# Kernel tuning notes

Measured on AMD Instinct MI355X. Metric: run time of the kernel, lower is better.

Reference implementation:

```python
import jax, jax.numpy as jnp
import numpy as np

B, S, D, H, FF = 4, 2048, 512, 8, 2048
W = 128  # local attention window size (hardcoded in module)
DH = D // H


def _ln(x, g, b, eps=1e-5):
    m = x.mean(-1, keepdims=True)
    v = ((x - m) ** 2).mean(-1, keepdims=True)
    return (x - m) / jnp.sqrt(v + eps) * g + b


def setup_inputs() -> dict:
    key = jax.random.key(0)
    ks = jax.random.split(key, 10)
    s = 0.02
    return {
        "src": jax.random.normal(ks[0], (B, S, D), jnp.float32),
        # global nn.MultiheadAttention params
        "in_proj_w": jax.random.normal(ks[1], (3 * D, D), jnp.float32) * s,
        "in_proj_b": jnp.zeros((3 * D,), jnp.float32),
        "out_proj_w": jax.random.normal(ks[2], (D, D), jnp.float32) * s,
        "out_proj_b": jnp.zeros((D,), jnp.float32),
        # LocalMHA params (prenorm LN, fused qkv no-bias, out proj no-bias)
        "ln_g": jnp.ones((D,), jnp.float32),
        "ln_b": jnp.zeros((D,), jnp.float32),
        "qkv_w": jax.random.normal(ks[3], (3 * D, D), jnp.float32) * s,
        "to_out_w": jax.random.normal(ks[4], (D, D), jnp.float32) * s,
        # glFusion + FFN + norms
        "gl_w": jax.random.normal(ks[5], (D, 2 * D), jnp.float32) * s,
        "gl_b": jnp.zeros((D,), jnp.float32),
        "norm1_g": jnp.ones((D,), jnp.float32),
        "norm1_b": jnp.zeros((D,), jnp.float32),
        "lin1_w": jax.random.normal(ks[6], (FF, D), jnp.float32) * s,
        "lin1_b": jnp.zeros((FF,), jnp.float32),
        "lin2_w": jax.random.normal(ks[7], (D, FF), jnp.float32) * s,
        "lin2_b": jnp.zeros((D,), jnp.float32),
        "norm2_g": jnp.ones((D,), jnp.float32),
        "norm2_b": jnp.zeros((D,), jnp.float32),
    }


def _forward(src, in_proj_w, in_proj_b, out_proj_w, out_proj_b, ln_g, ln_b,
             qkv_w, to_out_w, gl_w, gl_b, norm1_g, norm1_b,
             lin1_w, lin1_b, lin2_w, lin2_b, norm2_g, norm2_b):
    b, s, d = src.shape
    scale = DH ** -0.5

    def heads(x):  # (b, s, d) -> (b, H, s, DH)
        return x.reshape(b, s, H, DH).transpose(0, 2, 1, 3)

    # ---- global full MHA (no mask) ----
    qkv = src @ in_proj_w.T + in_proj_b
    qg, kg, vg = (heads(t) for t in jnp.split(qkv, 3, axis=-1))
    att = jax.nn.softmax(jnp.einsum('bhid,bhjd->bhij', qg, kg) * scale, axis=-1)
    go = jnp.einsum('bhij,bhjd->bhid', att, vg).transpose(0, 2, 1, 3).reshape(b, s, d)
    go = go @ out_proj_w.T + out_proj_b

    # ---- local windowed causal MHA with rotary (window=128, look_backward=1) ----
    x = _ln(src, ln_g, ln_b)  # prenorm
    ql, kl, vl = (heads(t) for t in jnp.split(x @ qkv_w.T, 3, axis=-1))

    pos = jnp.arange(s)
    inv_freq = 1.0 / (10000.0 ** (jnp.arange(0, DH, 2, dtype=jnp.float32) / DH))
    freqs = pos[:, None].astype(jnp.float32) * inv_freq[None, :]
    emb = jnp.concatenate([freqs, freqs], axis=-1)  # (s, DH)
    cos, sin = jnp.cos(emb), jnp.sin(emb)

    def rope(t):
        h = DH // 2
        t1, t2 = t[..., :h], t[..., h:]
        return t * cos + jnp.concatenate([-t2, t1], axis=-1) * sin

    ql, kl = rope(ql), rope(kl)
    ql = ql * scale

    nw = s // W
    qw = ql.reshape(b, H, nw, W, DH)
    kw = kl.reshape(b, H, nw, W, DH)
    vw = vl.reshape(b, H, nw, W, DH)

    def look_back(t):  # concat previous window with current: (b,H,nw,2W,DH)
        prev = jnp.pad(t, ((0, 0), (0, 0), (1, 0), (0, 0), (0, 0)))[:, :, :-1]
        return jnp.concatenate([prev, t], axis=3)

    bk, bv = look_back(kw), look_back(vw)

    qpos = pos.reshape(nw, W)
    kpos = jnp.concatenate(
        [jnp.concatenate([jnp.full((1, W), -1, pos.dtype), qpos[:-1]], axis=0), qpos],
        axis=1)  # (nw, 2W)
    mask = (kpos[:, None, :] >= 0) & (kpos[:, None, :] <= qpos[:, :, None])  # (nw,W,2W)

    sc = jnp.einsum('bhnid,bhnjd->bhnij', qw, bk)
    sc = jnp.where(mask, sc, jnp.finfo(sc.dtype).min)
    at = jax.nn.softmax(sc, axis=-1)
    lo = jnp.einsum('bhnij,bhnjd->bhnid', at, bv).reshape(b, H, s, DH)
    lo = lo.transpose(0, 2, 1, 3).reshape(b, s, d) @ to_out_w.T

    # ---- fuse global+local, residual, norms, FFN ----
    src2 = jnp.concatenate([go, lo], axis=-1) @ gl_w.T + gl_b
    h1 = _ln(src + src2, norm1_g, norm1_b)
    ff = jax.nn.relu(h1 @ lin1_w.T + lin1_b) @ lin2_w.T + lin2_b
    return _ln(h1 + ff, norm2_g, norm2_b)


def reference(src, in_proj_w, in_proj_b, out_proj_w, out_proj_b, ln_g, ln_b,
              qkv_w, to_out_w, gl_w, gl_b, norm1_g, norm1_b,
              lin1_w, lin1_b, lin2_w, lin2_b, norm2_g, norm2_b):
    return _forward(src, in_proj_w, in_proj_b, out_proj_w, out_proj_b, ln_g, ln_b,
                    qkv_w, to_out_w, gl_w, gl_b, norm1_g, norm1_b,
                    lin1_w, lin1_b, lin2_w, lin2_b, norm2_g, norm2_b)
```

## Files before the change

kernel.cpp:

```cpp
#include <hip/hip_runtime.h>
#include <math.h>

#define B_  4
#define S_  2048
#define D_  512
#define H_  8
#define FF_ 2048
#define W_  128
#define DH_ 64
#define TRD (3*D_)
#define MR_ (B_*S_)
#define QKLD 1024
#define SCQ 0.18033688011112042f

typedef __attribute__((ext_vector_type(8)))  short short8;
typedef __attribute__((ext_vector_type(4)))  float f32x4;
typedef __attribute__((ext_vector_type(16))) float f32x16;

__device__ __forceinline__ short f2bf(float f) {
    unsigned u = __float_as_uint(f);
    unsigned r = (u + 0x7fff + ((u >> 16) & 1)) >> 16;
    return (short)r;
}
__device__ __forceinline__ float bf2f(ushort u) {
    return __uint_as_float(((unsigned)u) << 16);
}
__device__ __forceinline__ unsigned pack_bf_trunc(float f0, float f1) {
    return __builtin_amdgcn_perm(__float_as_uint(f1), __float_as_uint(f0), 0x07060302u);
}
__device__ __forceinline__ void gload_lds16(const ushort* g, short* l) {
    __builtin_amdgcn_global_load_lds(
        (const __attribute__((address_space(1))) void*)g,
        (__attribute__((address_space(3))) void*)l, 16, 0, 0);
}

struct CvtJobs { const float* s[8]; ushort* d[8]; int n[8]; };

__global__ __launch_bounds__(256) void cvt_kernel(CvtJobs jobs)
{
    int i4 = (blockIdx.x * 256 + threadIdx.x) * 4;
    #pragma unroll
    for (int j = 0; j < 8; j++) {
        if (i4 < jobs.n[j]) {
            float4 v = *(const float4*)(jobs.s[j] + i4);
            ushort4 o;
            o.x = (ushort)f2bf(v.x); o.y = (ushort)f2bf(v.y);
            o.z = (ushort)f2bf(v.z); o.w = (ushort)f2bf(v.w);
            *(ushort4*)(jobs.d[j] + i4) = o;
        }
    }
}

__global__ __launch_bounds__(256) void gemm_bf16_kernel(
    const ushort* __restrict__ A, int lda,
    const ushort* __restrict__ Wt,
    const float* __restrict__ bias,
    ushort* __restrict__ C, int ldc,
    ushort* __restrict__ vt,
    int K, int relu)
{
    __shared__ short As[128 * 64];
    __shared__ short Bs[64 * 64];
    const int tid  = threadIdx.x;
    const int w    = tid >> 6;
    const int lane = tid & 63;
    const int quad = lane >> 4;
    const int x    = lane & 15;
    const int wr = w >> 1, wc = w & 1;
    const int bm = blockIdx.y * 128;
    const int bn = blockIdx.x * 64;

    const int srow = (lane >> 3);
    const int scol = ((lane & 7) ^ (lane >> 3)) * 8;

    f32x4 acc[4][2];
    #pragma unroll
    for (int i = 0; i < 4; i++)
        #pragma unroll
        for (int j = 0; j < 2; j++) acc[i][j] = (f32x4)0.f;

    for (int k0 = 0; k0 < K; k0 += 64) {
        __syncthreads();
        #pragma unroll
        for (int c = 0; c < 4; c++) {
            const ushort* ga = A + (size_t)(bm + w * 32 + c * 8 + srow) * lda + k0 + scol;
            gload_lds16(ga, &As[(w * 32 + c * 8) * 64]);
        }
        #pragma unroll
        for (int c = 0; c < 2; c++) {
            const ushort* gb = Wt + (size_t)(bn + w * 16 + c * 8 + srow) * K + k0 + scol;
            gload_lds16(gb, &Bs[(w * 16 + c * 8) * 64]);
        }
        __syncthreads();

        #pragma unroll
        for (int kc = 0; kc < 2; kc++) {
            short8 af[4], bf[2];
            int pcg = (kc * 4 + quad) ^ (x & 7);
            #pragma unroll
            for (int i = 0; i < 4; i++)
                af[i] = *(const short8*)&As[(wr * 64 + i * 16 + x) * 64 + pcg * 8];
            #pragma unroll
            for (int j = 0; j < 2; j++)
                bf[j] = *(const short8*)&Bs[(wc * 32 + j * 16 + x) * 64 + pcg * 8];
            #pragma unroll
            for (int i = 0; i < 4; i++)
                #pragma unroll
                for (int j = 0; j < 2; j++)
                    acc[i][j] = __builtin_amdgcn_mfma_f32_16x16x32_bf16(af[i], bf[j], acc[i][j], 0, 0, 0);
        }
    }

    if (vt) {
        #pragma unroll
        for (int i = 0; i < 4; i++) {
            int rowbase = bm + wr * 64 + i * 16 + quad * 4;
            #pragma unroll
            for (int j = 0; j < 2; j++) {
                int col = bn + wc * 32 + j * 16 + x;
                float bv = bias ? bias[col] : 0.f;
                if (col < 1024) {
                    #pragma unroll
                    for (int r = 0; r < 4; r++)
                        C[(size_t)(rowbase + r) * QKLD + col] = (ushort)f2bf(acc[i][j][r] + bv);
                } else {
                    int cv = col - 1024, hh = cv >> 6, dd = cv & 63;
                    int bb = rowbase >> 11, ss = rowbase & 2047;
                    int quadp = ((quad & 1) << 1) | (quad >> 1);
                    int sp = (ss & ~15) | (quadp << 2);
                    ushort4 p4;
                    p4.x = (ushort)f2bf(acc[i][j][0] + bv);
                    p4.y = (ushort)f2bf(acc[i][j][1] + bv);
                    p4.z = (ushort)f2bf(acc[i][j][2] + bv);
                    p4.w = (ushort)f2bf(acc[i][j][3] + bv);
                    *(ushort4*)(vt + ((size_t)((bb * 8 + hh) * 64 + dd)) * S_ + sp) = p4;
                }
            }
        }
    } else {
        #pragma unroll
        for (int i = 0; i < 4; i++) {
            #pragma unroll
            for (int r = 0; r < 4; r++) {
                size_t row = (size_t)(bm + wr * 64 + i * 16 + quad * 4 + r);
                #pragma unroll
                for (int j = 0; j < 2; j++) {
                    int col = bn + wc * 32 + j * 16 + x;
                    float v = acc[i][j][r] + (bias ? bias[col] : 0.f);
                    if (relu) v = v > 0.f ? v : 0.f;
                    C[row * ldc + col] = (ushort)f2bf(v);
                }
            }
        }
    }
}

__global__ __launch_bounds__(256) void gemm_bf16_splitk_kernel(
    const ushort* __restrict__ A, int lda,
    const ushort* __restrict__ Wt,
    float* __restrict__ P, int K)
{
    __shared__ short As[128 * 64];
    __shared__ short Bs[64 * 64];
    const int tid  = threadIdx.x;
    const int w    = tid >> 6;
    const int lane = tid & 63;
    const int quad = lane >> 4;
    const int x    = lane & 15;
    const int wr = w >> 1, wc = w & 1;
    const int bm = blockIdx.y * 128;
    const int bn = blockIdx.x * 64;
    const int kh = K >> 1;
    const int kbeg = blockIdx.z * kh;
    float* dst = P + (size_t)blockIdx.z * MR_ * D_;

    const int srow = (lane >> 3);
    const int scol = ((lane & 7) ^ (lane >> 3)) * 8;

    f32x4 acc[4][2];
    #pragma unroll
    for (int i = 0; i < 4; i++)
        #pragma unroll
        for (int j = 0; j < 2; j++) acc[i][j] = (f32x4)0.f;

    for (int k0 = kbeg; k0 < kbeg + kh; k0 += 64) {
        __syncthreads();
        #pragma unroll
        for (int c = 0; c < 4; c++) {
            const ushort* ga = A + (size_t)(bm + w * 32 + c * 8 + srow) * lda + k0 + scol;
            gload_lds16(ga, &As[(w * 32 + c * 8) * 64]);
        }
        #pragma unroll
        for (int c = 0; c < 2; c++) {
            const ushort* gb = Wt + (size_t)(bn + w * 16 + c * 8 + srow) * K + k0 + scol;
            gload_lds16(gb, &Bs[(w * 16 + c * 8) * 64]);
        }
        __syncthreads();

        #pragma unroll
        for (int kc = 0; kc < 2; kc++) {
            short8 af[4], bf[2];
            int pcg = (kc * 4 + quad) ^ (x & 7);
            #pragma unroll
            for (int i = 0; i < 4; i++)
                af[i] = *(const short8*)&As[(wr * 64 + i * 16 + x) * 64 + pcg * 8];
            #pragma unroll
            for (int j = 0; j < 2; j++)
                bf[j] = *(const short8*)&Bs[(wc * 32 + j * 16 + x) * 64 + pcg * 8];
            #pragma unroll
            for (int i = 0; i < 4; i++)
                #pragma unroll
                for (int j = 0; j < 2; j++)
                    acc[i][j] = __builtin_amdgcn_mfma_f32_16x16x32_bf16(af[i], bf[j], acc[i][j], 0, 0, 0);
        }
    }

    #pragma unroll
    for (int i = 0; i < 4; i++)
        #pragma unroll
        for (int r = 0; r < 4; r++) {
            size_t row = (size_t)(bm + wr * 64 + i * 16 + quad * 4 + r);
            #pragma unroll
            for (int j = 0; j < 2; j++) {
                int col = bn + wc * 32 + j * 16 + x;
                dst[row * D_ + col] = acc[i][j][r];
            }
        }
}

__device__ __forceinline__ float wave_sum64(float v) {
    #pragma unroll
    for (int off = 32; off > 0; off >>= 1) v += __shfl_xor(v, off, 64);
    return v;
}
__device__ __forceinline__ void load8(const float* p, float* v) {
    *(float4*)&v[0] = *(const float4*)p;
    *(float4*)&v[4] = *(const float4*)(p + 4);
}
__device__ __forceinline__ void load8(const ushort* p, float* v) {
    short8 s = *(const short8*)p;
    #pragma unroll
    for (int i = 0; i < 8; i++) v[i] = bf2f((ushort)s[i]);
}
__device__ __forceinline__ void store8(float* p, const float* v) {
    *(float4*)p       = make_float4(v[0], v[1], v[2], v[3]);
    *(float4*)(p + 4) = make_float4(v[4], v[5], v[6], v[7]);
}
__device__ __forceinline__ void store8(ushort* p, const float* v) {
    short8 s;
    #pragma unroll
    for (int i = 0; i < 8; i++) s[i] = f2bf(v[i]);
    *(short8*)p = s;
}
__device__ __forceinline__ void ln_core(float* v, int lane,
    const float* g, const float* be, float* t) {
    float s = 0.f;
    #pragma unroll
    for (int i = 0; i < 8; i++) s += v[i];
    float mean = wave_sum64(s) * (1.0f / 512.0f);
    float vs = 0.f;
    #pragma unroll
    for (int i = 0; i < 8; i++) { float d = v[i] - mean; vs += d * d; }
    float var = wave_sum64(vs) * (1.0f / 512.0f);
    float r = rsqrtf(var + 1e-5f);
    const int c = lane * 8;
    #pragma unroll
    for (int i = 0; i < 8; i++) t[i] = (v[i] - mean) * r * g[c + i] + be[c + i];
}

template <typename TA, typename TO>
__global__ __launch_bounds__(256) void addln_kernel(
    const TA* __restrict__ a,
    const float* __restrict__ g, const float* __restrict__ be,
    TO* __restrict__ out)
{
    const int lane = threadIdx.x & 63;
    const int row  = blockIdx.x * 4 + (threadIdx.x >> 6);
    const size_t base = (size_t)row * D_ + lane * 8;
    float v[8], t[8];
    load8(a + base, v);
    ln_core(v, lane, g, be, t);
    store8(out + base, t);
}

template <typename TA, typename TO>
__global__ __launch_bounds__(256) void ln_split_kernel(
    const TA* __restrict__ a,
    const float* __restrict__ p0, const float* __restrict__ p1,
    const float* __restrict__ bias,
    const float* __restrict__ g, const float* __restrict__ be,
    TO* __restrict__ out)
{
    const int lane = threadIdx.x & 63;
    const int row  = blockIdx.x * 4 + (threadIdx.x >> 6);
    const size_t base = (size_t)row * D_ + lane * 8;
    float v[8], w0[8], w1[8], t[8];
    load8(a + base, v);
    load8(p0 + base, w0);
    load8(p1 + base, w1);
    const int c = lane * 8;
    #pragma unroll
    for (int i = 0; i < 8; i++) v[i] += w0[i] + w1[i] + bias[c + i];
    ln_core(v, lane, g, be, t);
    store8(out + base, t);
}

__global__ __launch_bounds__(256) void transpose512_kernel(
    const ushort* __restrict__ in, ushort* __restrict__ out)
{
    __shared__ ushort T[64][72];
    const int t  = threadIdx.x;
    const int r0 = blockIdx.y * 64, c0 = blockIdx.x * 64;
    {
        int row = t >> 2, col = (t & 3) * 16;
        const ushort* s = in + (size_t)(r0 + row) * 512 + c0 + col;
        *(short8*)&T[row][col]     = *(const short8*)s;
        *(short8*)&T[row][col + 8] = *(const short8*)(s + 8);
    }
    __syncthreads();
    {
        int d = t >> 2, sc = (t & 3) * 16;
        ushort tmp[16];
        #pragma unroll
        for (int k = 0; k < 16; k++) tmp[k] = T[sc + k][d];
        ushort* dptr = out + (size_t)(c0 + d) * 512 + r0 + sc;
        *(short8*)dptr       = *(const short8*)&tmp[0];
        *(short8*)(dptr + 8) = *(const short8*)&tmp[8];
    }
}

__global__ __launch_bounds__(256) void fuse_bias_kernel(
    const float* __restrict__ gl_w, const float* __restrict__ opb,
    const float* __restrict__ gl_b, float* __restrict__ bf)
{
    const int lane = threadIdx.x & 63;
    const int row  = blockIdx.x * 4 + (threadIdx.x >> 6);
    float s = 0.f;
    #pragma unroll
    for (int i = 0; i < 8; i++) {
        int m = lane * 8 + i;
        s += gl_w[(size_t)row * 1024 + m] * opb[m];
    }
    s = wave_sum64(s);
    if (lane == 0) bf[row] = s + gl_b[row];
}

__global__ __launch_bounds__(256) void rope_kernel(ushort* __restrict__ qk)
{
    int idx = blockIdx.x * 256 + threadIdx.x;
    int d8 = idx & 3;
    int h  = (idx >> 2) & 7;
    int bs = idx >> 5;
    int pos = bs & (S_ - 1);
    ushort* base = qk + (size_t)bs * QKLD + h * 64 + d8 * 8;
    float q1[8], q2[8], k1[8], k2[8];
    load8(base, q1);       load8(base + 32, q2);
    load8(base + 512, k1); load8(base + 544, k2);
    float oq1[8], oq2[8], ok1[8], ok2[8];
    #pragma unroll
    for (int i = 0; i < 8; i++) {
        int d = d8 * 8 + i;
        float inv_freq = exp2f(-(float)d * (2.0f / 64.0f) * 13.287712379549449f);
        float ang = (float)pos * inv_freq;
        float sn, cs;
        __sincosf(ang, &sn, &cs);
        oq1[i] = (q1[i] * cs - q2[i] * sn) * SCQ;
        oq2[i] = (q2[i] * cs + q1[i] * sn) * SCQ;
        ok1[i] = k1[i] * cs - k2[i] * sn;
        ok2[i] = k2[i] * cs + k1[i] * sn;
    }
    store8(base, oq1);       store8(base + 32, oq2);
    store8(base + 512, ok1); store8(base + 544, ok2);
}

__global__ __launch_bounds__(256) void attn_kernel(
    const ushort* __restrict__ qkG, const ushort* __restrict__ vtG,
    const ushort* __restrict__ qkL, const ushort* __restrict__ vtL,
    ushort* __restrict__ cat)
{
    __shared__ short KsS[2][64 * 64];
    __shared__ short VtS[2][64 * 64];
    __shared__ float Lw[4][32];

    const int LOCAL = blockIdx.z;
    const ushort* qk = LOCAL ? qkL : qkG;
    const ushort* vt = LOCAL ? vtL : vtG;
    ushort* outp = cat + (LOCAL ? D_ : 0);

    const int tid  = threadIdx.x;
    const int w    = tid >> 6;
    const int lane = tid & 63;
    const int hl   = lane >> 5;
    const int c    = lane & 31;
    const int ks   = w >> 1;
    const int qh   = w & 1;
    const int bh = blockIdx.y;
    const int b = bh >> 3, h = bh & 7;
    const int qbase = blockIdx.x * 64;
    const int q0 = qbase + qh * 32;
    const size_t bS = (size_t)b * S_;
    const size_t vbase = (size_t)bh * DH_;

    short8 aq[4];
    {
        const ushort* qp = qk + (bS + q0 + c) * QKLD + h * 64;
        #pragma unroll
        for (int kc = 0; kc < 4; kc++) {
            short8 raw = *(const short8*)(qp + kc * 16 + hl * 8);
            if (LOCAL) aq[kc] = raw;
            else {
                #pragma unroll
                for (int j = 0; j < 8; j++) aq[kc][j] = f2bf(bf2f((ushort)raw[j]) * SCQ);
            }
        }
    }

    f32x16 ot[2];
    ot[0] = (f32x16)0.f; ot[1] = (f32x16)0.f;
    float lp = 0.f;

    const int NIT = LOCAL ? 2 : 16;
    for (int it = 0; it < NIT; it++) {
        const int tile  = ks * NIT + it;
        const int kbase = LOCAL ? ((qbase >> 7) * 128 - 128 + tile * 64) : tile * 64;
        const bool active = !LOCAL || (kbase >= 0 && kbase <= qbase + 63);
        __syncthreads();
        if (active) {
            #pragma unroll
            for (int cc = 0; cc < 4; cc++) {
                int row = qh * 32 + cc * 8 + (lane >> 3);
                int cg  = (lane & 7) ^ (lane >> 3);
                gload_lds16(qk + (bS + kbase + row) * QKLD + 512 + h * 64 + cg * 8,
                            &KsS[ks][(qh * 32 + cc * 8) * 64]);
                gload_lds16(vt + (vbase + row) * S_ + kbase + cg * 8,
                            &VtS[ks][(qh * 32 + cc * 8) * 64]);
            }
        }
        __syncthreads();
        if (!active) continue;
        const bool diag = LOCAL && (kbase == qbase);

        f32x16 e0 = (f32x16)0.f, e1 = (f32x16)0.f;
        #pragma unroll
        for (int kc = 0; kc < 4; kc++) {
            int pcg = (kc * 2 + hl) ^ (c & 7);
            short8 ak0 = *(const short8*)&KsS[ks][c * 64 + pcg * 8];
            e0 = __builtin_amdgcn_mfma_f32_32x32x16_bf16(ak0, aq[kc], e0, 0, 0, 0);
            short8 ak1 = *(const short8*)&KsS[ks][(32 + c) * 64 + pcg * 8];
            e1 = __builtin_amdgcn_mfma_f32_32x32x16_bf16(ak1, aq[kc], e1, 0, 0, 0);
        }

        const int qi = q0 + c;
        #pragma unroll
        for (int mt = 0; mt < 2; mt++) {
            f32x16& e = mt ? e1 : e0;
            #pragma unroll
            for (int r = 0; r < 16; r++) {
                float p = exp2f(e[r]);
                if (diag) {
                    int key = kbase + mt * 32 + (r & 3) + 8 * (r >> 2) + 4 * hl;
                    if (key > qi) p = 0.f;
                }
                e[r] = p;
                lp += p;
            }
        }

        #pragma unroll
        for (int t = 0; t < 4; t++) {
            const f32x16& e = (t < 2) ? e0 : e1;
            const int rb = 8 * (t & 1);
            uint4 u;
            u.x = pack_bf_trunc(e[rb + 0], e[rb + 1]);
            u.y = pack_bf_trunc(e[rb + 2], e[rb + 3]);
            u.z = pack_bf_trunc(e[rb + 4], e[rb + 5]);
            u.w = pack_bf_trunc(e[rb + 6], e[rb + 7]);
            short8 bp = *(short8*)&u;
            #pragma unroll
            for (int dt = 0; dt < 2; dt++) {
                int row = dt * 32 + c;
                int pcg = (t * 2 + hl) ^ (c & 7);
                short8 av = *(const short8*)&VtS[ks][row * 64 + pcg * 8];
                ot[dt] = __builtin_amdgcn_mfma_f32_32x32x16_bf16(av, bp, ot[dt], 0, 0, 0);
            }
        }
    }

    lp += __shfl_xor(lp, 32, 64);
    if (hl == 0) Lw[w][c] = lp;
    __syncthreads();

    float* scr = (float*)&KsS[0][0];
    if (w >= 2) {
        float* dst = scr + (w - 2) * 2048;
        #pragma unroll
        for (int dt = 0; dt < 2; dt++)
            #pragma unroll
            for (int r = 0; r < 16; r++)
                dst[(dt * 16 + r) * 64 + lane] = ot[dt][r];
    }
    __syncthreads();
    if (w < 2) {
        const float* srcp = scr + w * 2048;
        #pragma unroll
        for (int dt = 0; dt < 2; dt++)
            #pragma unroll
            for (int r = 0; r < 16; r++)
                ot[dt][r] += srcp[(dt * 16 + r) * 64 + lane];
        float inv = 1.0f / (Lw[w][c] + Lw[w + 2][c]);

        short* tr = (short*)&VtS[0][0] + w * 2304;
        #pragma unroll
        for (int dt = 0; dt < 2; dt++)
            #pragma unroll
            for (int rq = 0; rq < 4; rq++) {
                uint2 pkv;
                pkv.x = pack_bf_trunc(ot[dt][rq * 4 + 0] * inv, ot[dt][rq * 4 + 1] * inv);
                pkv.y = pack_bf_trunc(ot[dt][rq * 4 + 2] * inv, ot[dt][rq * 4 + 3] * inv);
                *(uint2*)&tr[c * 72 + dt * 32 + 8 * rq + 4 * hl] = pkv;
            }
        asm volatile("s_waitcnt lgkmcnt(0)" ::: "memory");
        __builtin_amdgcn_wave_barrier();
        {
            int q  = lane >> 1;
            int d0 = (lane & 1) * 32;
            short8 v0 = *(const short8*)&tr[q * 72 + d0];
            short8 v1 = *(const short8*)&tr[q * 72 + d0 + 8];
            short8 v2 = *(const short8*)&tr[q * 72 + d0 + 16];
            short8 v3 = *(const short8*)&tr[q * 72 + d0 + 24];
            ushort* op = outp + (bS + q0 + q) * 1024 + h * 64 + d0;
            *(short8*)(op)      = v0;
            *(short8*)(op + 8)  = v1;
            *(short8*)(op + 16) = v2;
            *(short8*)(op + 24) = v3;
        }
    }
}

extern "C" void kernel_launch(void* const* d_in, const int* in_sizes, int n_in,
                              void* d_out, int out_size, void* d_ws, size_t ws_size,
                              hipStream_t stream)
{
    (void)in_sizes; (void)n_in; (void)out_size; (void)ws_size;
    const float* src        = (const float*)d_in[0];
    const float* in_proj_w  = (const float*)d_in[1];
    const float* in_proj_b  = (const float*)d_in[2];
    const float* out_proj_w = (const float*)d_in[3];
    const float* out_proj_b = (const float*)d_in[4];
    const float* ln_g       = (const float*)d_in[5];
    const float* ln_b       = (const float*)d_in[6];
    const float* qkv_w      = (const float*)d_in[7];
    const float* to_out_w   = (const float*)d_in[8];
    const float* gl_w       = (const float*)d_in[9];
    const float* gl_b       = (const float*)d_in[10];
    const float* norm1_g    = (const float*)d_in[11];
    const float* norm1_b    = (const float*)d_in[12];
    const float* lin1_w     = (const float*)d_in[13];
    const float* lin1_b     = (const float*)d_in[14];
    const float* lin2_w     = (const float*)d_in[15];
    const float* lin2_b     = (const float*)d_in[16];
    const float* norm2_g    = (const float*)d_in[17];
    const float* norm2_b    = (const float*)d_in[18];
    float* out = (float*)d_out;

    ushort* ws16   = (ushort*)d_ws;
    ushort* src_bf = ws16;
    ushort* wi_bf  = src_bf + (size_t)MR_ * D_;
    ushort* wq_bf  = wi_bf  + TRD * D_;
    ushort* wo_bf  = wq_bf  + TRD * D_;
    ushort* wt_bf  = wo_bf  + D_ * D_;
    ushort* wg_bf  = wt_bf  + D_ * D_;
    ushort* w1_bf  = wg_bf  + D_ * 2 * D_;
    ushort* w2_bf  = w1_bf  + FF_ * D_;
    ushort* opwT   = w2_bf  + D_ * FF_;
    ushort* towT   = opwT   + D_ * D_;
    ushort* wcat   = towT   + D_ * D_;
    float*  bfuse  = (float*)(wcat + D_ * 2 * D_);
    ushort* buf1   = (ushort*)(bfuse + D_);
    ushort* h1b    = buf1 + (size_t)MR_ * D_;
    ushort* qkG    = h1b  + (size_t)MR_ * D_;
    ushort* vtg    = qkG  + (size_t)MR_ * QKLD;
    ushort* qkL    = vtg  + (size_t)MR_ * D_;
    ushort* vtl    = qkL  + (size_t)MR_ * QKLD;
    ushort* cat    = vtl  + (size_t)MR_ * D_;
    float*  part   = (float*)qkG;
    ushort* ff1    = qkL + (size_t)MR_ * D_;

    dim3 blk256(256);

    CvtJobs jobs;
    jobs.s[0] = src;        jobs.d[0] = src_bf; jobs.n[0] = MR_ * D_;
    jobs.s[1] = in_proj_w;  jobs.d[1] = wi_bf;  jobs.n[1] = TRD * D_;
    jobs.s[2] = qkv_w;      jobs.d[2] = wq_bf;  jobs.n[2] = TRD * D_;
    jobs.s[3] = out_proj_w; jobs.d[3] = wo_bf;  jobs.n[3] = D_ * D_;
    jobs.s[4] = to_out_w;   jobs.d[4] = wt_bf;  jobs.n[4] = D_ * D_;
    jobs.s[5] = gl_w;       jobs.d[5] = wg_bf;  jobs.n[5] = D_ * 2 * D_;
    jobs.s[6] = lin1_w;     jobs.d[6] = w1_bf;  jobs.n[6] = FF_ * D_;
    jobs.s[7] = lin2_w;     jobs.d[7] = w2_bf;  jobs.n[7] = D_ * FF_;
    cvt_kernel<<<dim3(4096), blk256, 0, stream>>>(jobs);

    transpose512_kernel<<<dim3(8, 8), blk256, 0, stream>>>(wo_bf, opwT);
    transpose512_kernel<<<dim3(8, 8), blk256, 0, stream>>>(wt_bf, towT);
    gemm_bf16_kernel<<<dim3(8, 4), blk256, 0, stream>>>(
        wg_bf, 2 * D_, opwT, nullptr, wcat, 2 * D_, nullptr, D_, 0);
    gemm_bf16_kernel<<<dim3(8, 4), blk256, 0, stream>>>(
        wg_bf + D_, 2 * D_, towT, nullptr, wcat + D_, 2 * D_, nullptr, D_, 0);
    fuse_bias_kernel<<<dim3(D_ / 4), blk256, 0, stream>>>(gl_w, out_proj_b, gl_b, bfuse);

    gemm_bf16_kernel<<<dim3(TRD / 64, MR_ / 128), blk256, 0, stream>>>(
        src_bf, D_, wi_bf, in_proj_b, qkG, QKLD, vtg, D_, 0);
    addln_kernel<float, ushort><<<dim3(MR_ / 4), blk256, 0, stream>>>(
        src, ln_g, ln_b, buf1);
    gemm_bf16_kernel<<<dim3(TRD / 64, MR_ / 128), blk256, 0, stream>>>(
        buf1, D_, wq_bf, nullptr, qkL, QKLD, vtl, D_, 0);
    rope_kernel<<<dim3((B_ * S_ * H_ * 4) / 256), blk256, 0, stream>>>(qkL);
    attn_kernel<<<dim3(S_ / 64, B_ * H_, 2), blk256, 0, stream>>>(
        qkG, vtg, qkL, vtl, cat);
    gemm_bf16_splitk_kernel<<<dim3(D_ / 64, MR_ / 128, 2), blk256, 0, stream>>>(
        cat, 2 * D_, wcat, part, 2 * D_);
    ln_split_kernel<float, ushort><<<dim3(MR_ / 4), blk256, 0, stream>>>(
        src, part, part + (size_t)MR_ * D_, bfuse, norm1_g, norm1_b, h1b);
    gemm_bf16_kernel<<<dim3(FF_ / 64, MR_ / 128), blk256, 0, stream>>>(
        h1b, D_, w1_bf, lin1_b, ff1, FF_, nullptr, D_, 1);
    gemm_bf16_splitk_kernel<<<dim3(D_ / 64, MR_ / 128, 2), blk256, 0, stream>>>(
        ff1, FF_, w2_bf, part, FF_);
    ln_split_kernel<ushort, float><<<dim3(MR_ / 4), blk256, 0, stream>>>(
        h1b, part, part + (size_t)MR_ * D_, lin2_b, norm2_g, norm2_b, out);
}
```

Measured before the change: 407.3 us.

## Widen GEMM tiles to 128x128 and specialize global attention loop

Both GEMM kernels now compute 128x128 output tiles per block instead of 128x64. Each wave holds a 4x4 MFMA accumulator set, and the A and B tile loads are merged into one loop. This doubles reuse of each A tile and halves grid sizes, at the cost of more registers and LDS and fewer blocks for the smaller GEMMs. The attention kernel also splits into separate global and local paths: the global path uses pointer increments with no active or diag checks, and row sums are split into two accumulators to shorten the dependency chain.

```diff
diff --git a/kernel.cpp b/kernel.cpp
--- a/kernel.cpp
+++ b/kernel.cpp
@@ -60,7 +60,7 @@
     int K, int relu)
 {
     __shared__ short As[128 * 64];
-    __shared__ short Bs[64 * 64];
+    __shared__ short Bs[128 * 64];
     const int tid  = threadIdx.x;
     const int w    = tid >> 6;
     const int lane = tid & 63;
@@ -68,45 +68,42 @@
     const int x    = lane & 15;
     const int wr = w >> 1, wc = w & 1;
     const int bm = blockIdx.y * 128;
-    const int bn = blockIdx.x * 64;
-
-    const int srow = (lane >> 3);
+    const int bn = blockIdx.x * 128;
+
+    const int srow = w * 32 + (lane >> 3);
     const int scol = ((lane & 7) ^ (lane >> 3)) * 8;
 
-    f32x4 acc[4][2];
+    f32x4 acc[4][4];
     #pragma unroll
     for (int i = 0; i < 4; i++)
         #pragma unroll
-        for (int j = 0; j < 2; j++) acc[i][j] = (f32x4)0.f;
+        for (int j = 0; j < 4; j++) acc[i][j] = (f32x4)0.f;
 
     for (int k0 = 0; k0 < K; k0 += 64) {
         __syncthreads();
         #pragma unroll
         for (int c = 0; c < 4; c++) {
-            const ushort* ga = A + (size_t)(bm + w * 32 + c * 8 + srow) * lda + k0 + scol;
+            const ushort* ga = A + (size_t)(bm + srow + c * 8) * lda + k0 + scol;
             gload_lds16(ga, &As[(w * 32 + c * 8) * 64]);
-        }
-        #pragma unroll
-        for (int c = 0; c < 2; c++) {
-            const ushort* gb = Wt + (size_t)(bn + w * 16 + c * 8 + srow) * K + k0 + scol;
-            gload_lds16(gb, &Bs[(w * 16 + c * 8) * 64]);
+            const ushort* gb = Wt + (size_t)(bn + srow + c * 8) * K + k0 + scol;
+            gload_lds16(gb, &Bs[(w * 32 + c * 8) * 64]);
         }
         __syncthreads();
 
         #pragma unroll
         for (int kc = 0; kc < 2; kc++) {
-            short8 af[4], bf[2];
+            short8 af[4], bf[4];
             int pcg = (kc * 4 + quad) ^ (x & 7);
             #pragma unroll
             for (int i = 0; i < 4; i++)
                 af[i] = *(const short8*)&As[(wr * 64 + i * 16 + x) * 64 + pcg * 8];
             #pragma unroll
-            for (int j = 0; j < 2; j++)
-                bf[j] = *(const short8*)&Bs[(wc * 32 + j * 16 + x) * 64 + pcg * 8];
+            for (int j = 0; j < 4; j++)
+                bf[j] = *(const short8*)&Bs[(wc * 64 + j * 16 + x) * 64 + pcg * 8];
             #pragma unroll
             for (int i = 0; i < 4; i++)
                 #pragma unroll
-                for (int j = 0; j < 2; j++)
+                for (int j = 0; j < 4; j++)
                     acc[i][j] = __builtin_amdgcn_mfma_f32_16x16x32_bf16(af[i], bf[j], acc[i][j], 0, 0, 0);
         }
     }
@@ -116,8 +113,8 @@
         for (int i = 0; i < 4; i++) {
             int rowbase = bm + wr * 64 + i * 16 + quad * 4;
             #pragma unroll
-            for (int j = 0; j < 2; j++) {
-                int col = bn + wc * 32 + j * 16 + x;
+            for (int j = 0; j < 4; j++) {
+                int col = bn + wc * 64 + j * 16 + x;
                 float bv = bias ? bias[col] : 0.f;
                 if (col < 1024) {
                     #pragma unroll
@@ -144,8 +141,8 @@
             for (int r = 0; r < 4; r++) {
                 size_t row = (size_t)(bm + wr * 64 + i * 16 + quad * 4 + r);
                 #pragma unroll
-                for (int j = 0; j < 2; j++) {
-                    int col = bn + wc * 32 + j * 16 + x;
+                for (int j = 0; j < 4; j++) {
+                    int col = bn + wc * 64 + j * 16 + x;
                     float v = acc[i][j][r] + (bias ? bias[col] : 0.f);
                     if (relu) v = v > 0.f ? v : 0.f;
                     C[row * ldc + col] = (ushort)f2bf(v);
@@ -161,7 +158,7 @@
     float* __restrict__ P, int K)
 {
     __shared__ short As[128 * 64];
-    __shared__ short Bs[64 * 64];
+    __shared__ short Bs[128 * 64];
     const int tid  = threadIdx.x;
     const int w    = tid >> 6;
     const int lane = tid & 63;
@@ -169,48 +166,45 @@
     const int x    = lane & 15;
     const int wr = w >> 1, wc = w & 1;
     const int bm = blockIdx.y * 128;
-    const int bn = blockIdx.x * 64;
+    const int bn = blockIdx.x * 128;
     const int kh = K >> 1;
     const int kbeg = blockIdx.z * kh;
     float* dst = P + (size_t)blockIdx.z * MR_ * D_;
 
-    const int srow = (lane >> 3);
+    const int srow = w * 32 + (lane >> 3);
     const int scol = ((lane & 7) ^ (lane >> 3)) * 8;
 
-    f32x4 acc[4][2];
+    f32x4 acc[4][4];
     #pragma unroll
     for (int i = 0; i < 4; i++)
         #pragma unroll
-        for (int j = 0; j < 2; j++) acc[i][j] = (f32x4)0.f;
+        for (int j = 0; j < 4; j++) acc[i][j] = (f32x4)0.f;
 
     for (int k0 = kbeg; k0 < kbeg + kh; k0 += 64) {
         __syncthreads();
         #pragma unroll
         for (int c = 0; c < 4; c++) {
-            const ushort* ga = A + (size_t)(bm + w * 32 + c * 8 + srow) * lda + k0 + scol;
+            const ushort* ga = A + (size_t)(bm + srow + c * 8) * lda + k0 + scol;
             gload_lds16(ga, &As[(w * 32 + c * 8) * 64]);
-        }
-        #pragma unroll
-        for (int c = 0; c < 2; c++) {
-            const ushort* gb = Wt + (size_t)(bn + w * 16 + c * 8 + srow) * K + k0 + scol;
-            gload_lds16(gb, &Bs[(w * 16 + c * 8) * 64]);
+            const ushort* gb = Wt + (size_t)(bn + srow + c * 8) * K + k0 + scol;
+            gload_lds16(gb, &Bs[(w * 32 + c * 8) * 64]);
         }
         __syncthreads();
 
         #pragma unroll
         for (int kc = 0; kc < 2; kc++) {
-            short8 af[4], bf[2];
+            short8 af[4], bf[4];
             int pcg = (kc * 4 + quad) ^ (x & 7);
             #pragma unroll
             for (int i = 0; i < 4; i++)
                 af[i] = *(const short8*)&As[(wr * 64 + i * 16 + x) * 64 + pcg * 8];
             #pragma unroll
-            for (int j = 0; j < 2; j++)
-                bf[j] = *(const short8*)&Bs[(wc * 32 + j * 16 + x) * 64 + pcg * 8];
+            for (int j = 0; j < 4; j++)
+                bf[j] = *(const short8*)&Bs[(wc * 64 + j * 16 + x) * 64 + pcg * 8];
             #pragma unroll
             for (int i = 0; i < 4; i++)
                 #pragma unroll
-                for (int j = 0; j < 2; j++)
+                for (int j = 0; j < 4; j++)
                     acc[i][j] = __builtin_amdgcn_mfma_f32_16x16x32_bf16(af[i], bf[j], acc[i][j], 0, 0, 0);
         }
     }
@@ -221,8 +215,8 @@
         for (int r = 0; r < 4; r++) {
             size_t row = (size_t)(bm + wr * 64 + i * 16 + quad * 4 + r);
             #pragma unroll
-            for (int j = 0; j < 2; j++) {
-                int col = bn + wc * 32 + j * 16 + x;
+            for (int j = 0; j < 4; j++) {
+                int col = bn + wc * 64 + j * 16 + x;
                 dst[row * D_ + col] = acc[i][j][r];
             }
         }
@@ -417,75 +411,133 @@
 
     f32x16 ot[2];
     ot[0] = (f32x16)0.f; ot[1] = (f32x16)0.f;
-    float lp = 0.f;
-
-    const int NIT = LOCAL ? 2 : 16;
-    for (int it = 0; it < NIT; it++) {
-        const int tile  = ks * NIT + it;
-        const int kbase = LOCAL ? ((qbase >> 7) * 128 - 128 + tile * 64) : tile * 64;
-        const bool active = !LOCAL || (kbase >= 0 && kbase <= qbase + 63);
-        __syncthreads();
-        if (active) {
+    float lpa = 0.f, lpb = 0.f;
+
+    const int rowk = qh * 32 + (lane >> 3);
+    const int cg   = (lane & 7) ^ (lane >> 3);
+    short* ldsk = &KsS[ks][(qh * 32) * 64];
+    short* ldsv = &VtS[ks][(qh * 32) * 64];
+
+    if (!LOCAL) {
+        const ushort* gk = qk + (bS + ks * 1024 + rowk) * QKLD + 512 + h * 64 + cg * 8;
+        const ushort* gv = vt + (vbase + rowk) * S_ + ks * 1024 + cg * 8;
+        for (int it = 0; it < 16; it++) {
+            __syncthreads();
             #pragma unroll
             for (int cc = 0; cc < 4; cc++) {
-                int row = qh * 32 + cc * 8 + (lane >> 3);
-                int cg  = (lane & 7) ^ (lane >> 3);
-                gload_lds16(qk + (bS + kbase + row) * QKLD + 512 + h * 64 + cg * 8,
-                            &KsS[ks][(qh * 32 + cc * 8) * 64]);
-                gload_lds16(vt + (vbase + row) * S_ + kbase + cg * 8,
-                            &VtS[ks][(qh * 32 + cc * 8) * 64]);
-            }
-        }
-        __syncthreads();
-        if (!active) continue;
-        const bool diag = LOCAL && (kbase == qbase);
-
-        f32x16 e0 = (f32x16)0.f, e1 = (f32x16)0.f;
-        #pragma unroll
-        for (int kc = 0; kc < 4; kc++) {
-            int pcg = (kc * 2 + hl) ^ (c & 7);
-            short8 ak0 = *(const short8*)&KsS[ks][c * 64 + pcg * 8];
-            e0 = __builtin_amdgcn_mfma_f32_32x32x16_bf16(ak0, aq[kc], e0, 0, 0, 0);
-            short8 ak1 = *(const short8*)&KsS[ks][(32 + c) * 64 + pcg * 8];
-            e1 = __builtin_amdgcn_mfma_f32_32x32x16_bf16(ak1, aq[kc], e1, 0, 0, 0);
-        }
-
-        const int qi = q0 + c;
-        #pragma unroll
-        for (int mt = 0; mt < 2; mt++) {
-            f32x16& e = mt ? e1 : e0;
-            #pragma unroll
-            for (int r = 0; r < 16; r++) {
-                float p = exp2f(e[r]);
-                if (diag) {
-                    int key = kbase + mt * 32 + (r & 3) + 8 * (r >> 2) + 4 * hl;
-                    if (key > qi) p = 0.f;
+                gload_lds16(gk + (size_t)(cc * 8) * QKLD, ldsk + cc * 8 * 64);
+                gload_lds16(gv + (size_t)(cc * 8) * S_,   ldsv + cc * 8 * 64);
+            }
+            __syncthreads();
+            gk += 64 * QKLD;
+            gv += 64;
+
+            f32x16 e0 = (f32x16)0.f, e1 = (f32x16)0.f;
+            #pragma unroll
+            for (int kc = 0; kc < 4; kc++) {
+                int pcg = (kc * 2 + hl) ^ (c & 7);
+                short8 ak0 = *(const short8*)&KsS[ks][c * 64 + pcg * 8];
+                e0 = __builtin_amdgcn_mfma_f32_32x32x16_bf16(ak0, aq[kc], e0, 0, 0, 0);
+                short8 ak1 = *(const short8*)&KsS[ks][(32 + c) * 64 + pcg * 8];
+                e1 = __builtin_amdgcn_mfma_f32_32x32x16_bf16(ak1, aq[kc], e1, 0, 0, 0);
+            }
+            #pragma unroll
+            for (int r = 0; r < 16; r++) { e0[r] = exp2f(e0[r]); }
+            #pragma unroll
+            for (int r = 0; r < 16; r++) { e1[r] = exp2f(e1[r]); }
+            #pragma unroll
+            for (int r = 0; r < 8; r++) {
+                lpa += e0[2 * r] + e1[2 * r];
+                lpb += e0[2 * r + 1] + e1[2 * r + 1];
+            }
+            #pragma unroll
+            for (int t = 0; t < 4; t++) {
+                const f32x16& e = (t < 2) ? e0 : e1;
+                const int rb = 8 * (t & 1);
+                uint4 u;
+                u.x = pack_bf_trunc(e[rb + 0], e[rb + 1]);
+                u.y = pack_bf_trunc(e[rb + 2], e[rb + 3]);
+                u.z = pack_bf_trunc(e[rb + 4], e[rb + 5]);
+                u.w = pack_bf_trunc(e[rb + 6], e[rb + 7]);
+                short8 bp = *(short8*)&u;
+                #pragma unroll
+                for (int dt = 0; dt < 2; dt++) {
+                    int row = dt * 32 + c;
+                    int pcg = (t * 2 + hl) ^ (c & 7);
+                    short8 av = *(const short8*)&VtS[ks][row * 64 + pcg * 8];
+                    ot[dt] = __builtin_amdgcn_mfma_f32_32x32x16_bf16(av, bp, ot[dt], 0, 0, 0);
                 }
-                e[r] = p;
-                lp += p;
-            }
-        }
-
-        #pragma unroll
-        for (int t = 0; t < 4; t++) {
-            const f32x16& e = (t < 2) ? e0 : e1;
-            const int rb = 8 * (t & 1);
-            uint4 u;
-            u.x = pack_bf_trunc(e[rb + 0], e[rb + 1]);
-            u.y = pack_bf_trunc(e[rb + 2], e[rb + 3]);
-            u.z = pack_bf_trunc(e[rb + 4], e[rb + 5]);
-            u.w = pack_bf_trunc(e[rb + 6], e[rb + 7]);
-            short8 bp = *(short8*)&u;
-            #pragma unroll
-            for (int dt = 0; dt < 2; dt++) {
-                int row = dt * 32 + c;
-                int pcg = (t * 2 + hl) ^ (c & 7);
-                short8 av = *(const short8*)&VtS[ks][row * 64 + pcg * 8];
-                ot[dt] = __builtin_amdgcn_mfma_f32_32x32x16_bf16(av, bp, ot[dt], 0, 0, 0);
-            }
-        }
-    }
-
+            }
+        }
+    } else {
+        for (int it = 0; it < 2; it++) {
+            const int tile  = ks * 2 + it;
+            const int kbase = (qbase >> 7) * 128 - 128 + tile * 64;
+            const bool active = (kbase >= 0 && kbase <= qbase + 63);
+            __syncthreads();
+            if (active) {
+                #pragma unroll
+                for (int cc = 0; cc < 4; cc++) {
+                    gload_lds16(qk + (bS + kbase + rowk + cc * 8) * QKLD + 512 + h * 64 + cg * 8,
+                                ldsk + cc * 8 * 64);
+                    gload_lds16(vt + (vbase + rowk + cc * 8) * S_ + kbase + cg * 8,
+                                ldsv + cc * 8 * 64);
+                }
+            }
+            __syncthreads();
+            if (!active) continue;
+            const bool diag = (kbase == qbase);
+
+            f32x16 e0 = (f32x16)0.f, e1 = (f32x16)0.f;
+            #pragma unroll
+            for (int kc = 0; kc < 4; kc++) {
+                int pcg = (kc * 2 + hl) ^ (c & 7);
+                short8 ak0 = *(const short8*)&KsS[ks][c * 64 + pcg * 8];
+                e0 = __builtin_amdgcn_mfma_f32_32x32x16_bf16(ak0, aq[kc], e0, 0, 0, 0);
+                short8 ak1 = *(const short8*)&KsS[ks][(32 + c) * 64 + pcg * 8];
+                e1 = __builtin_amdgcn_mfma_f32_32x32x16_bf16(ak1, aq[kc], e1, 0, 0, 0);
+            }
+            const int qi = q0 + c;
+            #pragma unroll
+            for (int mt = 0; mt < 2; mt++) {
+                f32x16& e = mt ? e1 : e0;
+                #pragma unroll
+                for (int r = 0; r < 16; r++) {
+                    float p = exp2f(e[r]);
+                    if (diag) {
+                        int key = kbase + mt * 32 + (r & 3) + 8 * (r >> 2) + 4 * hl;
+                        if (key > qi) p = 0.f;
+                    }
+                    e[r] = p;
+                }
+            }
+            #pragma unroll
+            for (int r = 0; r < 8; r++) {
+                lpa += e0[2 * r] + e1[2 * r];
+                lpb += e0[2 * r + 1] + e1[2 * r + 1];
+            }
+            #pragma unroll
+            for (int t = 0; t < 4; t++) {
+                const f32x16& e = (t < 2) ? e0 : e1;
+                const int rb = 8 * (t & 1);
+                uint4 u;
+                u.x = pack_bf_trunc(e[rb + 0], e[rb + 1]);
+                u.y = pack_bf_trunc(e[rb + 2], e[rb + 3]);
+                u.z = pack_bf_trunc(e[rb + 4], e[rb + 5]);
+                u.w = pack_bf_trunc(e[rb + 6], e[rb + 7]);
+                short8 bp = *(short8*)&u;
+                #pragma unroll
+                for (int dt = 0; dt < 2; dt++) {
+                    int row = dt * 32 + c;
+                    int pcg = (t * 2 + hl) ^ (c & 7);
+                    short8 av = *(const short8*)&VtS[ks][row * 64 + pcg * 8];
+                    ot[dt] = __builtin_amdgcn_mfma_f32_32x32x16_bf16(av, bp, ot[dt], 0, 0, 0);
+                }
+            }
+        }
+    }
+
+    float lp = lpa + lpb;
     lp += __shfl_xor(lp, 32, 64);
     if (hl == 0) Lw[w][c] = lp;
     __syncthreads();
@@ -601,28 +653,28 @@
 
     transpose512_kernel<<<dim3(8, 8), blk256, 0, stream>>>(wo_bf, opwT);
     transpose512_kernel<<<dim3(8, 8), blk256, 0, stream>>>(wt_bf, towT);
-    gemm_bf16_kernel<<<dim3(8, 4), blk256, 0, stream>>>(
+    gemm_bf16_kernel<<<dim3(4, 4), blk256, 0, stream>>>(
         wg_bf, 2 * D_, opwT, nullptr, wcat, 2 * D_, nullptr, D_, 0);
-    gemm_bf16_kernel<<<dim3(8, 4), blk256, 0, stream>>>(
+    gemm_bf16_kernel<<<dim3(4, 4), blk256, 0, stream>>>(
         wg_bf + D_, 2 * D_, towT, nullptr, wcat + D_, 2 * D_, nullptr, D_, 0);
     fuse_bias_kernel<<<dim3(D_ / 4), blk256, 0, stream>>>(gl_w, out_proj_b, gl_b, bfuse);
 
-    gemm_bf16_kernel<<<dim3(TRD / 64, MR_ / 128), blk256, 0, stream>>>(
+    gemm_bf16_kernel<<<dim3(TRD / 128, MR_ / 128), blk256, 0, stream>>>(
         src_bf, D_, wi_bf, in_proj_b, qkG, QKLD, vtg, D_, 0);
     addln_kernel<float, ushort><<<dim3(MR_ / 4), blk256, 0, stream>>>(
         src, ln_g, ln_b, buf1);
-    gemm_bf16_kernel<<<dim3(TRD / 64, MR_ / 128), blk256, 0, stream>>>(
+    gemm_bf16_kernel<<<dim3(TRD / 128, MR_ / 128), blk256, 0, stream>>>(
         buf1, D_, wq_bf, nullptr, qkL, QKLD, vtl, D_, 0);
     rope_kernel<<<dim3((B_ * S_ * H_ * 4) / 256), blk256, 0, stream>>>(qkL);
     attn_kernel<<<dim3(S_ / 64, B_ * H_, 2), blk256, 0, stream>>>(
         qkG, vtg, qkL, vtl, cat);
-    gemm_bf16_splitk_kernel<<<dim3(D_ / 64, MR_ / 128, 2), blk256, 0, stream>>>(
+    gemm_bf16_splitk_kernel<<<dim3(D_ / 128, MR_ / 128, 2), blk256, 0, stream>>>(
         cat, 2 * D_, wcat, part, 2 * D_);
     ln_split_kernel<float, ushort><<<dim3(MR_ / 4), blk256, 0, stream>>>(
         src, part, part + (size_t)MR_ * D_, bfuse, norm1_g, norm1_b, h1b);
-    gemm_bf16_kernel<<<dim3(FF_ / 64, MR_ / 128), blk256, 0, stream>>>(
+    gemm_bf16_kernel<<<dim3(FF_ / 128, MR_ / 128), blk256, 0, stream>>>(
         h1b, D_, w1_bf, lin1_b, ff1, FF_, nullptr, D_, 1);
-    gemm_bf16_splitk_kernel<<<dim3(D_ / 64, MR_ / 128, 2), blk256, 0, stream>>>(
+    gemm_bf16_splitk_kernel<<<dim3(D_ / 128, MR_ / 128, 2), blk256, 0, stream>>>(
         ff1, FF_, w2_bf, part, FF_);
     ln_split_kernel<ushort, float><<<dim3(MR_ / 4), blk256, 0, stream>>>(
         h1b, part, part + (size_t)MR_ * D_, lin2_b, norm2_g, norm2_b, out);
```

Measured after the change: 412.7 us. No clear change (+1.3%).
